# Optimization experiments

Hardware: AMD Instinct MI355X
Metric: run time of the kernel (lower is better)

Reference implementation:

```python
import jax, jax.numpy as jnp
import numpy as np
from jax import lax

K = 8          # num_classes
C_IN = 256     # in_channels
EPS = 1e-5


def resize_bilinear_ac(x, H, W):
    """Bilinear resize with align_corners=True. x: [B,C,h,w] -> [B,C,H,W]."""
    B, C, h, w = x.shape
    if h == H and w == W:
        return x
    ys = jnp.linspace(0.0, h - 1.0, H)
    xs = jnp.linspace(0.0, w - 1.0, W)
    y0 = jnp.floor(ys).astype(jnp.int32)
    x0 = jnp.floor(xs).astype(jnp.int32)
    y1 = jnp.minimum(y0 + 1, h - 1)
    x1 = jnp.minimum(x0 + 1, w - 1)
    wy = (ys - y0.astype(x.dtype))[None, None, :, None]
    wx = (xs - x0.astype(x.dtype))[None, None, None, :]
    g00 = x[:, :, y0][:, :, :, x0]
    g01 = x[:, :, y0][:, :, :, x1]
    g10 = x[:, :, y1][:, :, :, x0]
    g11 = x[:, :, y1][:, :, :, x1]
    top = g00 * (1.0 - wx) + g01 * wx
    bot = g10 * (1.0 - wx) + g11 * wx
    return top * (1.0 - wy) + bot * wy


def setup_inputs() -> dict:
    key = jax.random.key(0)
    ks = jax.random.split(key, 16)
    shapes = [(2, 256, 128, 128), (2, 256, 64, 64), (2, 256, 32, 32), (2, 256, 16, 16), (2, 256, 8, 8)]
    inp = {}
    for i, s in enumerate(shapes):
        inp[f"feat{i}"] = jax.random.normal(ks[i], s, dtype=jnp.float32)
    inp["attr_feat"] = jax.random.normal(ks[5], (2, K * C_IN, 64, 64), dtype=jnp.float32)
    # learned params
    inp["mlp_f_w"] = jax.random.normal(ks[6], (256, 256), dtype=jnp.float32) * 0.02
    inp["mlp_f_b"] = jnp.zeros((256,), dtype=jnp.float32)
    inp["mlp_a_w"] = jax.random.normal(ks[7], (256, 256), dtype=jnp.float32) * 0.02
    inp["mlp_a_b"] = jnp.zeros((256,), dtype=jnp.float32)
    # 5 grouped convs: [out=2048, in_per_group=256, 3, 3] each, no bias (BN follows)
    inp["conv_w"] = jax.random.normal(ks[8], (5, K * C_IN, C_IN, 3, 3), dtype=jnp.float32) * 0.02
    inp["bn_gamma"] = jnp.ones((5, K * C_IN), dtype=jnp.float32)
    inp["bn_beta"] = jnp.zeros((5, K * C_IN), dtype=jnp.float32)
    inp["bn_mean"] = jax.random.normal(ks[9], (5, K * C_IN), dtype=jnp.float32) * 0.1
    inp["bn_var"] = jax.random.uniform(ks[10], (5, K * C_IN), dtype=jnp.float32, minval=0.5, maxval=1.5)
    return inp


def _forward(feats, attr_feat, mlp_f_w, mlp_f_b, mlp_a_w, mlp_a_b, conv_w, bn_gamma, bn_beta, bn_mean, bn_var):
    B = attr_feat.shape[0]
    # global avg pool attr -> [B, K, C] -> mlp_a
    avg_attr = attr_feat.mean(axis=(2, 3)).reshape(B, K, C_IN)
    avg_attr = avg_attr @ mlp_a_w.T + mlp_a_b  # [B,K,256]
    outs = []
    for i, x in enumerate(feats):
        _, C, H, W = x.shape
        avg_x = x.mean(axis=(2, 3)) @ mlp_f_w.T + mlp_f_b          # [B,256]
        logits = jnp.einsum('bkc,bc->bk', avg_attr, avg_x)          # [B,K]
        attn = jax.nn.softmax(logits, axis=-1)
        y = resize_bilinear_ac(attr_feat, H, W)                      # [B,2048,H,W]
        y = lax.conv_general_dilated(
            y, conv_w[i], window_strides=(1, 1), padding=((1, 1), (1, 1)),
            dimension_numbers=('NCHW', 'OIHW', 'NCHW'), feature_group_count=K)
        inv = lax.rsqrt(bn_var[i] + EPS)
        y = (y - bn_mean[i][None, :, None, None]) * (inv * bn_gamma[i])[None, :, None, None] + bn_beta[i][None, :, None, None]
        y = jax.nn.relu(y)
        y = y.reshape(B, K, C, H, W)
        y = jnp.einsum('bkchw,bk->bchw', y, attn)                   # weighted sum over classes
        outs.append(jax.nn.relu(x + y))
    return tuple(outs)


def reference(feat0, feat1, feat2, feat3, feat4, attr_feat, mlp_f_w, mlp_f_b, mlp_a_w, mlp_a_b, conv_w, bn_gamma, bn_beta, bn_mean, bn_var):
    feats = [feat0, feat1, feat2, feat3, feat4]
    return _forward(feats, attr_feat, mlp_f_w, mlp_f_b, mlp_a_w, mlp_a_b, conv_w, bn_gamma, bn_beta, bn_mean, bn_var)
```

## Files before the change

kernel.cpp:

```cpp
#include <hip/hip_runtime.h>
#include <hip/hip_bf16.h>
#include <cstdint>

typedef __attribute__((ext_vector_type(8))) short short8;
typedef __attribute__((ext_vector_type(4))) float f32x4;

#define EPSV 1e-5f

__device__ __forceinline__ void gload_lds16(const void* g, void* l) {
  __builtin_amdgcn_global_load_lds(
      (const __attribute__((address_space(1))) void*)(uintptr_t)g,
      (__attribute__((address_space(3))) void*)(uint32_t)(uintptr_t)l,
      16, 0, 0);
}

__global__ void mean_kernel(const float* __restrict__ in, float* __restrict__ out,
                            int HW, float inv) {
  const int ch = blockIdx.x;
  const int t = threadIdx.x;
  const float* p = in + (size_t)ch * HW;
  float s = 0.f;
  const int nv = HW >> 2;
  const float4* pv = (const float4*)p;
  for (int i = t; i < nv; i += 256) { float4 v = pv[i]; s += v.x + v.y + v.z + v.w; }
  __shared__ float red[256];
  red[t] = s; __syncthreads();
  for (int off = 128; off > 0; off >>= 1) {
    if (t < off) red[t] += red[t + off];
    __syncthreads();
  }
  if (t == 0) out[ch] = red[0] * inv;
}

__global__ void wtrans_kernel(const float* __restrict__ cw,
                              const float* __restrict__ gamma, const float* __restrict__ beta,
                              const float* __restrict__ mean, const float* __restrict__ var,
                              __hip_bfloat16* __restrict__ wt, float* __restrict__ bias) {
  const int oc = blockIdx.x;
  const int i  = blockIdx.y;
  const int ci = threadIdx.x;
  const int idx = i * 2048 + oc;
  const float sc = rsqrtf(var[idx] + EPSV) * gamma[idx];
  if (ci == 0) bias[idx] = beta[idx] - mean[idx] * sc;
  const int g = oc >> 8, co = oc & 255;
  const float* src = cw + ((size_t)idx * 256 + ci) * 9;
  const size_t dbase = (size_t)(i * 8 + g) * 9 * 65536 + co * 256 + ci;
#pragma unroll
  for (int tap = 0; tap < 9; ++tap)
    wt[dbase + (size_t)tap * 65536] = __float2bfloat16(src[tap] * sc);
}

__global__ void gate_kernel(const float* __restrict__ meanA, const float* __restrict__ meanF,
                            const float* __restrict__ Wa, const float* __restrict__ ba,
                            const float* __restrict__ Wf, const float* __restrict__ bfp,
                            float* __restrict__ attn) {
  __shared__ float mA[16 * 256];
  __shared__ float mF[10 * 256];
  __shared__ float pA[16 * 256];
  __shared__ float pF[10 * 256];
  __shared__ float lg[80];
  const int t = threadIdx.x;
  for (int i = t; i < 4096; i += 256) mA[i] = meanA[i];
  for (int i = t; i < 2560; i += 256) mF[i] = meanF[i];
  __syncthreads();
  {
    float acc[16];
#pragma unroll
    for (int j = 0; j < 16; ++j) acc[j] = 0.f;
    for (int ci = 0; ci < 256; ++ci) {
      const float w = Wa[t * 256 + ci];
#pragma unroll
      for (int j = 0; j < 16; ++j) acc[j] += mA[j * 256 + ci] * w;
    }
    const float bb = ba[t];
#pragma unroll
    for (int j = 0; j < 16; ++j) pA[j * 256 + t] = acc[j] + bb;
  }
  {
    float acc[10];
#pragma unroll
    for (int j = 0; j < 10; ++j) acc[j] = 0.f;
    for (int ci = 0; ci < 256; ++ci) {
      const float w = Wf[t * 256 + ci];
#pragma unroll
      for (int j = 0; j < 10; ++j) acc[j] += mF[j * 256 + ci] * w;
    }
    const float bb = bfp[t];
#pragma unroll
    for (int j = 0; j < 10; ++j) pF[j * 256 + t] = acc[j] + bb;
  }
  __syncthreads();
  if (t < 80) {
    const int i = t >> 4, r = t & 15, b = r >> 3, k = r & 7;
    const float* a = &pA[(b * 8 + k) * 256];
    const float* f = &pF[(i * 2 + b) * 256];
    float d = 0.f;
    for (int c = 0; c < 256; ++c) d += a[c] * f[c];
    lg[t] = d;
  }
  __syncthreads();
  if (t < 10) {
    const int base = t * 8;
    float m = lg[base];
    for (int k = 1; k < 8; ++k) m = fmaxf(m, lg[base + k]);
    float e[8], s = 0.f;
    for (int k = 0; k < 8; ++k) { e[k] = __expf(lg[base + k] - m); s += e[k]; }
    const float invs = 1.f / s;
    for (int k = 0; k < 8; ++k) attn[base + k] = e[k] * invs;
  }
}

__global__ void resize_kernel(const float* __restrict__ attr,
                              __hip_bfloat16* __restrict__ R,
                              int W, int Hp, int Wp, float scl) {
  const int bk = blockIdx.x;
  const int yp = blockIdx.y;
  const int t  = threadIdx.x;
  const size_t rowbase = ((size_t)bk * Hp + yp) * (size_t)Wp * 256;
  if (yp == 0 || yp == Hp - 1) {
    uint32_t* p = (uint32_t*)(R + rowbase);
    const int n = Wp * 128;
    for (int idx = t; idx < n; idx += 256) p[idx] = 0u;
    return;
  }
  const int y = yp - 1;
  const float fy = y * scl;
  int y0 = (int)floorf(fy); if (y0 > 63) y0 = 63;
  const float wy = fy - (float)y0;
  const int y1 = min(y0 + 1, 63);
  __shared__ float buf[2][64][65];
  const int cc = t >> 2, seg = (t & 3) * 16;
  const int bb = bk >> 3, k = bk & 7;
  const float* ab = attr + (size_t)bb * 2048 * 4096;
  const int ci = t & 63;
  for (int cq = 0; cq < 4; ++cq) {
    __syncthreads();
    {
      const int ch = k * 256 + cq * 64 + cc;
      const float* r0 = ab + ((size_t)ch * 64 + y0) * 64;
      const float* r1 = ab + ((size_t)ch * 64 + y1) * 64;
#pragma unroll
      for (int u = 0; u < 4; ++u) {
        float4 v0 = ((const float4*)r0)[(t & 3) * 4 + u];
        float4 v1 = ((const float4*)r1)[(t & 3) * 4 + u];
        buf[0][cc][seg + u * 4 + 0] = v0.x; buf[0][cc][seg + u * 4 + 1] = v0.y;
        buf[0][cc][seg + u * 4 + 2] = v0.z; buf[0][cc][seg + u * 4 + 3] = v0.w;
        buf[1][cc][seg + u * 4 + 0] = v1.x; buf[1][cc][seg + u * 4 + 1] = v1.y;
        buf[1][cc][seg + u * 4 + 2] = v1.z; buf[1][cc][seg + u * 4 + 3] = v1.w;
      }
    }
    __syncthreads();
    for (int x = t >> 6; x < W; x += 4) {
      const float fx = x * scl;
      int x0 = (int)floorf(fx); if (x0 > 63) x0 = 63;
      const float wx = fx - (float)x0;
      const int x1 = min(x0 + 1, 63);
      const float top = buf[0][ci][x0] * (1.f - wx) + buf[0][ci][x1] * wx;
      const float bot = buf[1][ci][x0] * (1.f - wx) + buf[1][ci][x1] * wx;
      R[rowbase + (size_t)(x + 1) * 256 + cq * 64 + ci] = __float2bfloat16(top * (1.f - wy) + bot * wy);
    }
    if (t < 64) {
      R[rowbase + cq * 64 + t] = __float2bfloat16(0.f);
      R[rowbase + (size_t)(Wp - 1) * 256 + cq * 64 + t] = __float2bfloat16(0.f);
    }
  }
}

__device__ __forceinline__ void coords36(int u, int g0, int& g, int& ty, int& tx, int& cq) {
  g = g0 + u / 36;
  const int r = u % 36;
  const int tap = r >> 2;
  cq = r & 3;
  ty = tap / 3;
  tx = tap - ty * 3;
}

__global__ __launch_bounds__(256, 2)
void conv_kernel(const __hip_bfloat16* __restrict__ R,
                 const __hip_bfloat16* __restrict__ Wt,
                 const float* __restrict__ bias,
                 const float* __restrict__ attn,
                 const float* __restrict__ featp,
                 float* __restrict__ outp,
                 int W, int lw, int Hp, int Wp, int HW,
                 int b0, int NB, int gcount) {
  __shared__ alignas(16) __hip_bfloat16 ldsA[2][128 * 64];
  __shared__ alignas(16) __hip_bfloat16 ldsB[3][128 * 64];
  const int tid  = threadIdx.x;
  const int lane = tid & 63;
  const int wave = __builtin_amdgcn_readfirstlane(tid >> 6);
  const int wm = (wave >> 1) * 64;
  const int wn = (wave & 1) * 64;

  const int nx  = gridDim.x;
  const int lin = blockIdx.x;
  const int pos = ((nx & 7) == 0) ? ((lin & 7) * (nx >> 3) + (lin >> 3)) : lin;
  const int co0 = (pos & 1) * 128;
  const int n0  = (pos >> 1) * 128;

  const int bb  = (int)blockIdx.y % NB;
  const int gs  = (int)blockIdx.y / NB;
  const int b   = b0 + bb;
  const int g0  = gs * gcount;

  const int c8 = lane & 7;
  const int r8 = lane >> 3;
  int aoff[4], boff[4], dst[4];
#pragma unroll
  for (int q = 0; q < 4; ++q) {
    const int row = (wave * 4 + q) * 8 + r8;
    const int sc = (c8 ^ (row & 7)) << 3;
    aoff[q] = ((co0 + row) << 8) + sc;
    int sg = n0 + row; if (sg >= HW) sg = HW - 1;
    const int y = sg >> lw, x = sg & (W - 1);
    boff[q] = ((y * Wp + x) << 8) + sc;
    dst[q] = (wave * 4 + q) * 512;
  }

  const size_t rgstride = (size_t)Hp * Wp * 256;
  const __hip_bfloat16* Rb = R + (size_t)bb * 8 * rgstride;

  const f32x4 fz = {0.f, 0.f, 0.f, 0.f};
  f32x4 fin[4][4], acc[4][4];
#pragma unroll
  for (int mf = 0; mf < 4; ++mf)
#pragma unroll
    for (int nf = 0; nf < 4; ++nf) { fin[mf][nf] = fz; acc[mf][nf] = fz; }

  const int nstages = gcount * 36;

  {
    int g, ty, tx, cq;
    coords36(0, g0, g, ty, tx, cq);
    const __hip_bfloat16* wp = Wt + (((size_t)g * 9 + ty * 3 + tx) << 16) + (cq << 6);
    const __hip_bfloat16* rp = Rb + (size_t)g * rgstride + ((ty * Wp + tx) << 8) + (cq << 6);
#pragma unroll
    for (int q = 0; q < 4; ++q) gload_lds16(wp + aoff[q], &ldsA[0][dst[q]]);
#pragma unroll
    for (int q = 0; q < 4; ++q) gload_lds16(rp + boff[q], &ldsB[0][dst[q]]);
    coords36(1, g0, g, ty, tx, cq);
    const __hip_bfloat16* rp1 = Rb + (size_t)g * rgstride + ((ty * Wp + tx) << 8) + (cq << 6);
#pragma unroll
    for (int q = 0; q < 4; ++q) gload_lds16(rp1 + boff[q], &ldsB[1][dst[q]]);
  }

  int bcur = 0, b2 = 2;
  int foldc = 0, gcur = g0;

  for (int s = 0; s < nstages; ++s) {
    __builtin_amdgcn_s_barrier();
    asm volatile("" ::: "memory");
    if (s + 1 < nstages) {
      int g, ty, tx, cq;
      coords36(s + 1, g0, g, ty, tx, cq);
      const __hip_bfloat16* wp = Wt + (((size_t)g * 9 + ty * 3 + tx) << 16) + (cq << 6);
      __hip_bfloat16* dA = &ldsA[(s + 1) & 1][0];
#pragma unroll
      for (int q = 0; q < 4; ++q) gload_lds16(wp + aoff[q], dA + dst[q]);
    }
    if (s + 2 < nstages) {
      int g, ty, tx, cq;
      coords36(s + 2, g0, g, ty, tx, cq);
      const __hip_bfloat16* rp = Rb + (size_t)g * rgstride + ((ty * Wp + tx) << 8) + (cq << 6);
      __hip_bfloat16* dB = &ldsB[b2][0];
#pragma unroll
      for (int q = 0; q < 4; ++q) gload_lds16(rp + boff[q], dB + dst[q]);
    }
    if (s + 2 < nstages)      asm volatile("s_waitcnt vmcnt(12)" ::: "memory");
    else if (s + 1 < nstages) asm volatile("s_waitcnt vmcnt(8)" ::: "memory");
    else                      asm volatile("s_waitcnt vmcnt(0)" ::: "memory");
    __builtin_amdgcn_s_barrier();
    asm volatile("" ::: "memory");

    const __hip_bfloat16* pA = &ldsA[s & 1][0];
    const __hip_bfloat16* pB = &ldsB[bcur][0];
#pragma unroll
    for (int ks = 0; ks < 2; ++ks) {
      short8 af[4], bfv[4];
      const int cb = ks * 4 + (lane >> 4);
#pragma unroll
      for (int mf = 0; mf < 4; ++mf) {
        const int row = wm + mf * 16 + (lane & 15);
        af[mf] = *(const short8*)&pA[(row << 6) + ((cb ^ (row & 7)) << 3)];
      }
#pragma unroll
      for (int nf = 0; nf < 4; ++nf) {
        const int row = wn + nf * 16 + (lane & 15);
        bfv[nf] = *(const short8*)&pB[(row << 6) + ((cb ^ (row & 7)) << 3)];
      }
#pragma unroll
      for (int mf = 0; mf < 4; ++mf)
#pragma unroll
        for (int nf = 0; nf < 4; ++nf)
          acc[mf][nf] = __builtin_amdgcn_mfma_f32_16x16x32_bf16(
              af[mf], bfv[nf], acc[mf][nf], 0, 0, 0);
    }

    if (++bcur == 3) bcur = 0;
    if (++b2 == 3) b2 = 0;

    if (++foldc == 36) {
      foldc = 0;
      const float aw = attn[b * 8 + gcur];
#pragma unroll
      for (int mf = 0; mf < 4; ++mf) {
        const int cobase = co0 + wm + mf * 16 + ((lane >> 4) << 2);
#pragma unroll
        for (int r = 0; r < 4; ++r) {
          const float bs = bias[(gcur << 8) + cobase + r];
#pragma unroll
          for (int nf = 0; nf < 4; ++nf) {
            fin[mf][nf][r] += aw * fmaxf(acc[mf][nf][r] + bs, 0.f);
            acc[mf][nf][r] = 0.f;
          }
        }
      }
      ++gcur;
    }
  }

  const size_t plane = (size_t)256 * HW;
  if (featp) {
    const float* fb = featp + (size_t)b * plane;
    float* ob = outp + (size_t)b * plane;
#pragma unroll
    for (int mf = 0; mf < 4; ++mf) {
      const int cobase = co0 + wm + mf * 16 + ((lane >> 4) << 2);
#pragma unroll
      for (int nf = 0; nf < 4; ++nf) {
        const int n = n0 + wn + nf * 16 + (lane & 15);
        if (n < HW) {
#pragma unroll
          for (int r = 0; r < 4; ++r) {
            const size_t idx = (size_t)(cobase + r) * HW + n;
            ob[idx] = fmaxf(fb[idx] + fin[mf][nf][r], 0.f);
          }
        }
      }
    }
  } else {
    float* zb = outp + ((size_t)gs * 2 + b) * plane;
#pragma unroll
    for (int mf = 0; mf < 4; ++mf) {
      const int cobase = co0 + wm + mf * 16 + ((lane >> 4) << 2);
#pragma unroll
      for (int nf = 0; nf < 4; ++nf) {
        const int n = n0 + wn + nf * 16 + (lane & 15);
        if (n < HW) {
#pragma unroll
          for (int r = 0; r < 4; ++r)
            zb[(size_t)(cobase + r) * HW + n] = fin[mf][nf][r];
        }
      }
    }
  }
}

__global__ void reduce_kernel(const float* __restrict__ z, const float* __restrict__ feat,
                              float* __restrict__ outp, int total, int S) {
  const int idx = blockIdx.x * 256 + threadIdx.x;
  if (idx >= total) return;
  float s = feat[idx];
  for (int j = 0; j < S; ++j) s += z[(size_t)j * total + idx];
  outp[idx] = fmaxf(s, 0.f);
}

extern "C" void kernel_launch(void* const* d_in, const int* in_sizes, int n_in,
                              void* d_out, int out_size, void* d_ws, size_t ws_size,
                              hipStream_t stream) {
  const float* feat[5];
  for (int i = 0; i < 5; ++i) feat[i] = (const float*)d_in[i];
  const float* attr = (const float*)d_in[5];
  const float* mfw = (const float*)d_in[6];
  const float* mfb = (const float*)d_in[7];
  const float* maw = (const float*)d_in[8];
  const float* mab = (const float*)d_in[9];
  const float* cw  = (const float*)d_in[10];
  const float* bng = (const float*)d_in[11];
  const float* bnb = (const float*)d_in[12];
  const float* bnm = (const float*)d_in[13];
  const float* bnv = (const float*)d_in[14];
  float* out = (float*)d_out;

  char* ws = (char*)d_ws;
  float* attnW = (float*)(ws);
  float* meanA = (float*)(ws + 512);
  float* meanF = (float*)(ws + 20480);
  float* biasW = (float*)(ws + 32768);
  __hip_bfloat16* Wt = (__hip_bfloat16*)(ws + 131072);
  const size_t R_OFF = 47316992;
  __hip_bfloat16* Rbuf = (__hip_bfloat16*)(ws + R_OFF);

  const bool full = ws_size >= (size_t)219316224;
  const int NB = full ? 2 : 1;
  float* zbuf = (float*)(ws + R_OFF + (size_t)NB * 69222400);

  static const int HS[5] = {128, 64, 32, 16, 8};
  static const size_t OOFF[5] = {0, 8388608, 10485760, 11010048, 11141120};
  static const int SPLIT[5] = {1, 4, 8, 8, 8};

  mean_kernel<<<4096, 256, 0, stream>>>(attr, meanA, 4096, 1.f / 4096.f);
  for (int i = 0; i < 5; ++i) {
    const int HW = HS[i] * HS[i];
    mean_kernel<<<512, 256, 0, stream>>>(feat[i], meanF + i * 512, HW, 1.f / (float)HW);
  }
  wtrans_kernel<<<dim3(2048, 5), 256, 0, stream>>>(cw, bng, bnb, bnm, bnv, Wt, biasW);
  gate_kernel<<<1, 256, 0, stream>>>(meanA, meanF, maw, mab, mfw, mfb, attnW);

  for (int i = 0; i < 5; ++i) {
    const int H = HS[i], W = H, HW = H * W, Hp = H + 2, Wp = W + 2;
    const int lw = 31 - __builtin_clz((unsigned)W);
    const float scl = 63.f / (float)(H - 1);
    const int S = full ? SPLIT[i] : 1;
    const int gcount = 8 / S;
    const int ntiles = (HW + 127) / 128;
    for (int b0 = 0; b0 < 2; b0 += NB) {
      resize_kernel<<<dim3(NB * 8, Hp), 256, 0, stream>>>(
          attr + (size_t)b0 * 2048 * 4096, Rbuf, W, Hp, Wp, scl);
      const float* fp = (S == 1) ? feat[i] : nullptr;
      float* op = (S == 1) ? (out + OOFF[i]) : zbuf;
      conv_kernel<<<dim3(ntiles * 2, NB * S), 256, 0, stream>>>(
          Rbuf, Wt + (size_t)i * 8 * 9 * 65536, biasW + i * 2048, attnW + i * 16,
          fp, op, W, lw, Hp, Wp, HW, b0, NB, gcount);
    }
    if (S > 1) {
      const int total = 2 * 256 * HW;
      reduce_kernel<<<(total + 255) / 256, 256, 0, stream>>>(zbuf, feat[i], out + OOFF[i], total, S);
    }
  }
}
```

Baseline: 742.6 us.

## Load conv weight fragments straight into registers, double-buffer activation LDS

The weight (A) operand no longer goes through LDS. Each wave loads its MFMA A-fragments directly from global memory into registers with inline global_load_dwordx4, ping-ponging between two register sets across an unrolled pair of stages. The activation (B) tile drops from triple- to double-buffered LDS with a one-stage prefetch. This removes LDS traffic and footprint for A, but raises register pressure and leaves global latency hidden by only one stage of lookahead.

```diff
diff --git a/kernel.cpp b/kernel.cpp
--- a/kernel.cpp
+++ b/kernel.cpp
@@ -12,6 +12,14 @@
       (const __attribute__((address_space(1))) void*)(uintptr_t)g,
       (__attribute__((address_space(3))) void*)(uint32_t)(uintptr_t)l,
       16, 0, 0);
+}
+
+template <int OFF>
+__device__ __forceinline__ short8 aload(const __hip_bfloat16* sbase, uint32_t voff) {
+  short8 d;
+  asm volatile("global_load_dwordx4 %0, %1, %2 offset:%3"
+               : "=v"(d) : "v"(voff), "s"(sbase), "i"(OFF));
+  return d;
 }
 
 __global__ void mean_kernel(const float* __restrict__ in, float* __restrict__ out,
@@ -184,8 +192,7 @@
                  float* __restrict__ outp,
                  int W, int lw, int Hp, int Wp, int HW,
                  int b0, int NB, int gcount) {
-  __shared__ alignas(16) __hip_bfloat16 ldsA[2][128 * 64];
-  __shared__ alignas(16) __hip_bfloat16 ldsB[3][128 * 64];
+  __shared__ alignas(16) __hip_bfloat16 ldsB[2][128 * 64];
   const int tid  = threadIdx.x;
   const int lane = tid & 63;
   const int wave = __builtin_amdgcn_readfirstlane(tid >> 6);
@@ -205,17 +212,17 @@
 
   const int c8 = lane & 7;
   const int r8 = lane >> 3;
-  int aoff[4], boff[4], dst[4];
+  int boff[4], dst[4];
 #pragma unroll
   for (int q = 0; q < 4; ++q) {
     const int row = (wave * 4 + q) * 8 + r8;
     const int sc = (c8 ^ (row & 7)) << 3;
-    aoff[q] = ((co0 + row) << 8) + sc;
     int sg = n0 + row; if (sg >= HW) sg = HW - 1;
     const int y = sg >> lw, x = sg & (W - 1);
     boff[q] = ((y * Wp + x) << 8) + sc;
     dst[q] = (wave * 4 + q) * 512;
   }
+  const uint32_t voff = ((uint32_t)(co0 + wm + (lane & 15)) << 9) + ((lane >> 4) << 4);
 
   const size_t rgstride = (size_t)Hp * Wp * 256;
   const __hip_bfloat16* Rb = R + (size_t)bb * 8 * rgstride;
@@ -228,78 +235,71 @@
     for (int nf = 0; nf < 4; ++nf) { fin[mf][nf] = fz; acc[mf][nf] = fz; }
 
   const int nstages = gcount * 36;
+  short8 aP[8], aQ[8];
 
   {
-    int g, ty, tx, cq;
-    coords36(0, g0, g, ty, tx, cq);
-    const __hip_bfloat16* wp = Wt + (((size_t)g * 9 + ty * 3 + tx) << 16) + (cq << 6);
-    const __hip_bfloat16* rp = Rb + (size_t)g * rgstride + ((ty * Wp + tx) << 8) + (cq << 6);
-#pragma unroll
-    for (int q = 0; q < 4; ++q) gload_lds16(wp + aoff[q], &ldsA[0][dst[q]]);
+    const __hip_bfloat16* rp = Rb + (size_t)g0 * rgstride;
 #pragma unroll
     for (int q = 0; q < 4; ++q) gload_lds16(rp + boff[q], &ldsB[0][dst[q]]);
-    coords36(1, g0, g, ty, tx, cq);
-    const __hip_bfloat16* rp1 = Rb + (size_t)g * rgstride + ((ty * Wp + tx) << 8) + (cq << 6);
-#pragma unroll
-    for (int q = 0; q < 4; ++q) gload_lds16(rp1 + boff[q], &ldsB[1][dst[q]]);
-  }
-
-  int bcur = 0, b2 = 2;
+    const __hip_bfloat16* sA = Wt + ((size_t)g0 * 9 << 16);
+#pragma unroll
+    for (int mf = 0; mf < 4; ++mf) {
+      aP[mf * 2 + 0] = aload<0>(sA + mf * 4096, voff);
+      aP[mf * 2 + 1] = aload<64>(sA + mf * 4096, voff);
+    }
+  }
+
   int foldc = 0, gcur = g0;
 
-  for (int s = 0; s < nstages; ++s) {
-    __builtin_amdgcn_s_barrier();
-    asm volatile("" ::: "memory");
-    if (s + 1 < nstages) {
-      int g, ty, tx, cq;
-      coords36(s + 1, g0, g, ty, tx, cq);
-      const __hip_bfloat16* wp = Wt + (((size_t)g * 9 + ty * 3 + tx) << 16) + (cq << 6);
-      __hip_bfloat16* dA = &ldsA[(s + 1) & 1][0];
-#pragma unroll
-      for (int q = 0; q < 4; ++q) gload_lds16(wp + aoff[q], dA + dst[q]);
-    }
-    if (s + 2 < nstages) {
-      int g, ty, tx, cq;
-      coords36(s + 2, g0, g, ty, tx, cq);
-      const __hip_bfloat16* rp = Rb + (size_t)g * rgstride + ((ty * Wp + tx) << 8) + (cq << 6);
-      __hip_bfloat16* dB = &ldsB[b2][0];
-#pragma unroll
-      for (int q = 0; q < 4; ++q) gload_lds16(rp + boff[q], dB + dst[q]);
-    }
-    if (s + 2 < nstages)      asm volatile("s_waitcnt vmcnt(12)" ::: "memory");
-    else if (s + 1 < nstages) asm volatile("s_waitcnt vmcnt(8)" ::: "memory");
-    else                      asm volatile("s_waitcnt vmcnt(0)" ::: "memory");
-    __builtin_amdgcn_s_barrier();
-    asm volatile("" ::: "memory");
-
-    const __hip_bfloat16* pA = &ldsA[s & 1][0];
-    const __hip_bfloat16* pB = &ldsB[bcur][0];
-#pragma unroll
-    for (int ks = 0; ks < 2; ++ks) {
-      short8 af[4], bfv[4];
-      const int cb = ks * 4 + (lane >> 4);
-#pragma unroll
-      for (int mf = 0; mf < 4; ++mf) {
-        const int row = wm + mf * 16 + (lane & 15);
-        af[mf] = *(const short8*)&pA[(row << 6) + ((cb ^ (row & 7)) << 3)];
-      }
-#pragma unroll
-      for (int nf = 0; nf < 4; ++nf) {
-        const int row = wn + nf * 16 + (lane & 15);
-        bfv[nf] = *(const short8*)&pB[(row << 6) + ((cb ^ (row & 7)) << 3)];
-      }
-#pragma unroll
-      for (int mf = 0; mf < 4; ++mf)
-#pragma unroll
-        for (int nf = 0; nf < 4; ++nf)
-          acc[mf][nf] = __builtin_amdgcn_mfma_f32_16x16x32_bf16(
-              af[mf], bfv[nf], acc[mf][nf], 0, 0, 0);
-    }
-
-    if (++bcur == 3) bcur = 0;
-    if (++b2 == 3) b2 = 0;
-
-    if (++foldc == 36) {
+#define STAGE(s_, AUSE, ALOAD)                                                 \
+  {                                                                            \
+    __builtin_amdgcn_s_barrier();                                              \
+    asm volatile("" ::: "memory");                                             \
+    if ((s_) + 1 < nstages) {                                                  \
+      int g1, ty1, tx1, cq1;                                                   \
+      coords36((s_) + 1, g0, g1, ty1, tx1, cq1);                               \
+      const __hip_bfloat16* rp = Rb + (size_t)g1 * rgstride +                  \
+                                 ((ty1 * Wp + tx1) << 8) + (cq1 << 6);         \
+      __hip_bfloat16* dB = &ldsB[((s_) + 1) & 1][0];                           \
+      _Pragma("unroll")                                                        \
+      for (int q = 0; q < 4; ++q) gload_lds16(rp + boff[q], dB + dst[q]);      \
+      const __hip_bfloat16* sA =                                               \
+          Wt + (((size_t)g1 * 9 + ty1 * 3 + tx1) << 16) + (cq1 << 6);          \
+      _Pragma("unroll")                                                        \
+      for (int mf = 0; mf < 4; ++mf) {                                         \
+        ALOAD[mf * 2 + 0] = aload<0>(sA + mf * 4096, voff);                    \
+        ALOAD[mf * 2 + 1] = aload<64>(sA + mf * 4096, voff);                   \
+      }                                                                        \
+      asm volatile("s_waitcnt vmcnt(12)" ::: "memory");                        \
+    } else {                                                                   \
+      asm volatile("s_waitcnt vmcnt(0)" ::: "memory");                         \
+    }                                                                          \
+    __builtin_amdgcn_s_barrier();                                              \
+    asm volatile("" ::: "memory");                                             \
+    const __hip_bfloat16* pB = &ldsB[(s_) & 1][0];                             \
+    _Pragma("unroll")                                                          \
+    for (int ks = 0; ks < 2; ++ks) {                                           \
+      short8 bfv[4];                                                           \
+      const int cb = ks * 4 + (lane >> 4);                                     \
+      _Pragma("unroll")                                                        \
+      for (int nf = 0; nf < 4; ++nf) {                                         \
+        const int row = wn + nf * 16 + (lane & 15);                            \
+        bfv[nf] = *(const short8*)&pB[(row << 6) + ((cb ^ (row & 7)) << 3)];   \
+      }                                                                        \
+      _Pragma("unroll")                                                        \
+      for (int mf = 0; mf < 4; ++mf)                                           \
+        _Pragma("unroll")                                                      \
+        for (int nf = 0; nf < 4; ++nf)                                         \
+          acc[mf][nf] = __builtin_amdgcn_mfma_f32_16x16x32_bf16(               \
+              AUSE[mf * 2 + ks], bfv[nf], acc[mf][nf], 0, 0, 0);               \
+    }                                                                          \
+  }
+
+  for (int s = 0; s < nstages; s += 2) {
+    STAGE(s, aP, aQ);
+    STAGE(s + 1, aQ, aP);
+    foldc += 2;
+    if (foldc == 36) {
       foldc = 0;
       const float aw = attn[b * 8 + gcur];
 #pragma unroll
@@ -318,6 +318,7 @@
       ++gcur;
     }
   }
+#undef STAGE
 
   const size_t plane = (size_t)256 * HW;
   if (featp) {
```

Measured after the change: 1.136 ms. 53.0% more time.

## Add 256x256-tile conv kernel for large levels with bf16 split-K partials

Applied to the files above, without the earlier changes.

Adds a 512-thread conv kernel using 256x256 output tiles (all 256 output channels per block) with interleaved LDS prefetch, setprio around MFMA bursts, and accumulators folded into packed bf16 registers. It is used for the two largest pyramid levels with a class-group split (2 or 8), while smaller levels keep the old kernel split 8 ways. Split partial sums are now stored as bf16 instead of fp32, and the reduce kernel is vectorized over four elements per thread. This aims to raise arithmetic intensity per loaded tile and cut partial-sum traffic, at the cost of precision loss from bf16 intermediate accumulation and higher register pressure.

```diff
diff --git a/kernel.cpp b/kernel.cpp
--- a/kernel.cpp
+++ b/kernel.cpp
@@ -12,6 +12,12 @@
       (const __attribute__((address_space(1))) void*)(uintptr_t)g,
       (__attribute__((address_space(3))) void*)(uint32_t)(uintptr_t)l,
       16, 0, 0);
+}
+
+__device__ __forceinline__ uint32_t f2bf_rne(float v) {
+  const uint32_t u = __float_as_uint(v);
+  const uint32_t r = ((u >> 16) & 1u) + 0x7fffu;
+  return (u + r) >> 16;
 }
 
 __global__ void mean_kernel(const float* __restrict__ in, float* __restrict__ out,
@@ -175,13 +181,179 @@
   tx = tap - ty * 3;
 }
 
+__global__ __launch_bounds__(512, 1)
+void conv256_kernel(const __hip_bfloat16* __restrict__ R,
+                    const __hip_bfloat16* __restrict__ Wt,
+                    const float* __restrict__ bias,
+                    const float* __restrict__ attn,
+                    __hip_bfloat16* __restrict__ zout,
+                    int W, int lw, int Hp, int Wp, int HW,
+                    int NB, int gcount) {
+  __shared__ alignas(16) __hip_bfloat16 ldsA[2][256 * 64];
+  __shared__ alignas(16) __hip_bfloat16 ldsB[2][256 * 64];
+  const int tid  = threadIdx.x;
+  const int lane = tid & 63;
+  const int wave = __builtin_amdgcn_readfirstlane(tid >> 6);
+  const int wm = (wave >> 2) * 128;
+  const int wn = (wave & 3) * 64;
+
+  const int nx  = gridDim.x;
+  const int lin = blockIdx.x;
+  const int pos = ((nx & 7) == 0) ? ((lin & 7) * (nx >> 3) + (lin >> 3)) : lin;
+  const int n0  = pos * 256;
+
+  const int bb = (int)blockIdx.y % NB;
+  const int gs = (int)blockIdx.y / NB;
+  const int g0 = gs * gcount;
+
+  const int c8 = lane & 7, r8 = lane >> 3;
+  const int sc = (c8 ^ r8) << 3;
+  const int aoff0 = ((wave * 32 + r8) << 8) + sc;
+  const int dst0  = wave * 2048;
+  int boff[4];
+#pragma unroll
+  for (int q = 0; q < 4; ++q) {
+    const int row = wave * 32 + q * 8 + r8;
+    const int sg = n0 + row;
+    const int y = sg >> lw, x = sg & (W - 1);
+    boff[q] = ((y * Wp + x) << 8) + sc;
+  }
+
+  const size_t rgstride = (size_t)Hp * Wp * 256;
+  const __hip_bfloat16* Rb = R + (size_t)bb * 8 * rgstride;
+
+  const f32x4 fz = {0.f, 0.f, 0.f, 0.f};
+  f32x4 acc[8][4];
+  uint32_t finp[8][4][2];
+#pragma unroll
+  for (int mf = 0; mf < 8; ++mf)
+#pragma unroll
+    for (int nf = 0; nf < 4; ++nf) {
+      acc[mf][nf] = fz; finp[mf][nf][0] = 0u; finp[mf][nf][1] = 0u;
+    }
+
+  const int nk = gcount * 36;
+  {
+    const __hip_bfloat16* wp = Wt + ((size_t)g0 * 9 << 16);
+    const __hip_bfloat16* rp = Rb + (size_t)g0 * rgstride;
+#pragma unroll
+    for (int q = 0; q < 4; ++q) gload_lds16(wp + aoff0 + q * 2048, &ldsA[0][dst0 + q * 512]);
+#pragma unroll
+    for (int q = 0; q < 4; ++q) gload_lds16(rp + boff[q], &ldsB[0][dst0 + q * 512]);
+  }
+
+  int foldc = 0, gcur = g0;
+  for (int t = 0; t < nk; ++t) {
+    const int c = t & 1;
+    const bool pf = (t + 1 < nk);
+    int g1, ty1, tx1, cq1;
+    coords36(pf ? t + 1 : t, g0, g1, ty1, tx1, cq1);
+    const __hip_bfloat16* wp1 = Wt + (((size_t)g1 * 9 + ty1 * 3 + tx1) << 16) + (cq1 << 6);
+    const __hip_bfloat16* rp1 = Rb + (size_t)g1 * rgstride + ((ty1 * Wp + tx1) << 8) + (cq1 << 6);
+
+    asm volatile("s_waitcnt vmcnt(0)" ::: "memory");
+    __builtin_amdgcn_s_barrier();
+    asm volatile("" ::: "memory");
+
+    const __hip_bfloat16* pA = &ldsA[c][0];
+    const __hip_bfloat16* pB = &ldsB[c][0];
+    __hip_bfloat16* dA = &ldsA[c ^ 1][0];
+    __hip_bfloat16* dB = &ldsB[c ^ 1][0];
+
+#pragma unroll
+    for (int ks = 0; ks < 2; ++ks) {
+      const int cb = ks * 4 + (lane >> 4);
+      short8 bfv[4];
+#pragma unroll
+      for (int nf = 0; nf < 4; ++nf) {
+        const int row = wn + nf * 16 + (lane & 15);
+        bfv[nf] = *(const short8*)&pB[(row << 6) + ((cb ^ (row & 7)) << 3)];
+      }
+#pragma unroll
+      for (int h = 0; h < 2; ++h) {
+        short8 af[4];
+#pragma unroll
+        for (int m = 0; m < 4; ++m) {
+          const int row = wm + (h * 4 + m) * 16 + (lane & 15);
+          af[m] = *(const short8*)&pA[(row << 6) + ((cb ^ (row & 7)) << 3)];
+        }
+        if (ks == 0 && pf) {
+          if (h == 0) {
+#pragma unroll
+            for (int q = 0; q < 4; ++q) gload_lds16(wp1 + aoff0 + q * 2048, dA + dst0 + q * 512);
+          } else {
+#pragma unroll
+            for (int q = 0; q < 4; ++q) gload_lds16(rp1 + boff[q], dB + dst0 + q * 512);
+          }
+        }
+        __builtin_amdgcn_s_barrier();
+        __builtin_amdgcn_sched_barrier(0);
+        __builtin_amdgcn_s_setprio(1);
+#pragma unroll
+        for (int m = 0; m < 4; ++m)
+#pragma unroll
+          for (int nf = 0; nf < 4; ++nf)
+            acc[h * 4 + m][nf] = __builtin_amdgcn_mfma_f32_16x16x32_bf16(
+                af[m], bfv[nf], acc[h * 4 + m][nf], 0, 0, 0);
+        __builtin_amdgcn_s_setprio(0);
+        __builtin_amdgcn_s_barrier();
+        asm volatile("" ::: "memory");
+      }
+    }
+
+    if (++foldc == 36) {
+      foldc = 0;
+      const float aw = attn[bb * 8 + gcur];
+#pragma unroll
+      for (int mf = 0; mf < 8; ++mf) {
+        const int cobase = wm + mf * 16 + ((lane >> 4) << 2);
+#pragma unroll
+        for (int pr = 0; pr < 2; ++pr) {
+          const float b0v = bias[(gcur << 8) + cobase + pr * 2 + 0];
+          const float b1v = bias[(gcur << 8) + cobase + pr * 2 + 1];
+#pragma unroll
+          for (int nf = 0; nf < 4; ++nf) {
+            const uint32_t p = finp[mf][nf][pr];
+            const float f0 = __uint_as_float(p << 16)
+                           + aw * fmaxf(acc[mf][nf][pr * 2 + 0] + b0v, 0.f);
+            const float f1 = __uint_as_float(p & 0xffff0000u)
+                           + aw * fmaxf(acc[mf][nf][pr * 2 + 1] + b1v, 0.f);
+            finp[mf][nf][pr] = (f2bf_rne(f1) << 16) | f2bf_rne(f0);
+          }
+        }
+#pragma unroll
+        for (int nf = 0; nf < 4; ++nf) acc[mf][nf] = fz;
+      }
+      ++gcur;
+    }
+  }
+
+  __hip_bfloat16* zb = zout + (size_t)(gs * 2 + bb) * 256 * (size_t)HW;
+#pragma unroll
+  for (int mf = 0; mf < 8; ++mf) {
+    const int cobase = wm + mf * 16 + ((lane >> 4) << 2);
+#pragma unroll
+    for (int nf = 0; nf < 4; ++nf) {
+      const int n = n0 + wn + nf * 16 + (lane & 15);
+#pragma unroll
+      for (int pr = 0; pr < 2; ++pr) {
+        const uint32_t p = finp[mf][nf][pr];
+        zb[(size_t)(cobase + pr * 2 + 0) * HW + n] =
+            __float2bfloat16(__uint_as_float(p << 16));
+        zb[(size_t)(cobase + pr * 2 + 1) * HW + n] =
+            __float2bfloat16(__uint_as_float(p & 0xffff0000u));
+      }
+    }
+  }
+}
+
 __global__ __launch_bounds__(256, 2)
 void conv_kernel(const __hip_bfloat16* __restrict__ R,
                  const __hip_bfloat16* __restrict__ Wt,
                  const float* __restrict__ bias,
                  const float* __restrict__ attn,
                  const float* __restrict__ featp,
-                 float* __restrict__ outp,
+                 void* __restrict__ outp,
                  int W, int lw, int Hp, int Wp, int HW,
                  int b0, int NB, int gcount) {
   __shared__ alignas(16) __hip_bfloat16 ldsA[2][128 * 64];
@@ -228,7 +400,6 @@
     for (int nf = 0; nf < 4; ++nf) { fin[mf][nf] = fz; acc[mf][nf] = fz; }
 
   const int nstages = gcount * 36;
-
   {
     int g, ty, tx, cq;
     coords36(0, g0, g, ty, tx, cq);
@@ -238,7 +409,7 @@
     for (int q = 0; q < 4; ++q) gload_lds16(wp + aoff[q], &ldsA[0][dst[q]]);
 #pragma unroll
     for (int q = 0; q < 4; ++q) gload_lds16(rp + boff[q], &ldsB[0][dst[q]]);
-    coords36(1, g0, g, ty, tx, cq);
+    coords36(1 < nstages ? 1 : 0, g0, g, ty, tx, cq);
     const __hip_bfloat16* rp1 = Rb + (size_t)g * rgstride + ((ty * Wp + tx) << 8) + (cq << 6);
 #pragma unroll
     for (int q = 0; q < 4; ++q) gload_lds16(rp1 + boff[q], &ldsB[1][dst[q]]);
@@ -322,7 +493,7 @@
   const size_t plane = (size_t)256 * HW;
   if (featp) {
     const float* fb = featp + (size_t)b * plane;
-    float* ob = outp + (size_t)b * plane;
+    float* ob = (float*)outp + (size_t)b * plane;
 #pragma unroll
     for (int mf = 0; mf < 4; ++mf) {
       const int cobase = co0 + wm + mf * 16 + ((lane >> 4) << 2);
@@ -339,7 +510,7 @@
       }
     }
   } else {
-    float* zb = outp + ((size_t)gs * 2 + b) * plane;
+    __hip_bfloat16* zb = (__hip_bfloat16*)outp + ((size_t)gs * 2 + b) * plane;
 #pragma unroll
     for (int mf = 0; mf < 4; ++mf) {
       const int cobase = co0 + wm + mf * 16 + ((lane >> 4) << 2);
@@ -349,20 +520,29 @@
         if (n < HW) {
 #pragma unroll
           for (int r = 0; r < 4; ++r)
-            zb[(size_t)(cobase + r) * HW + n] = fin[mf][nf][r];
+            zb[(size_t)(cobase + r) * HW + n] = __float2bfloat16(fin[mf][nf][r]);
         }
       }
     }
   }
 }
 
-__global__ void reduce_kernel(const float* __restrict__ z, const float* __restrict__ feat,
+__global__ void reduce_kernel(const __hip_bfloat16* __restrict__ z,
+                              const float* __restrict__ feat,
                               float* __restrict__ outp, int total, int S) {
-  const int idx = blockIdx.x * 256 + threadIdx.x;
-  if (idx >= total) return;
-  float s = feat[idx];
-  for (int j = 0; j < S; ++j) s += z[(size_t)j * total + idx];
-  outp[idx] = fmaxf(s, 0.f);
+  const int i4 = (blockIdx.x * 256 + threadIdx.x) * 4;
+  if (i4 >= total) return;
+  float4 f = *(const float4*)(feat + i4);
+  float s0 = f.x, s1 = f.y, s2 = f.z, s3 = f.w;
+  for (int j = 0; j < S; ++j) {
+    const ushort4 v = *(const ushort4*)(z + (size_t)j * total + i4);
+    s0 += __uint_as_float((uint32_t)v.x << 16);
+    s1 += __uint_as_float((uint32_t)v.y << 16);
+    s2 += __uint_as_float((uint32_t)v.z << 16);
+    s3 += __uint_as_float((uint32_t)v.w << 16);
+  }
+  float4 o = {fmaxf(s0, 0.f), fmaxf(s1, 0.f), fmaxf(s2, 0.f), fmaxf(s3, 0.f)};
+  *(float4*)(outp + i4) = o;
 }
 
 extern "C" void kernel_launch(void* const* d_in, const int* in_sizes, int n_in,
@@ -393,11 +573,10 @@
 
   const bool full = ws_size >= (size_t)219316224;
   const int NB = full ? 2 : 1;
-  float* zbuf = (float*)(ws + R_OFF + (size_t)NB * 69222400);
+  __hip_bfloat16* zbuf = (__hip_bfloat16*)(ws + R_OFF + (size_t)NB * 69222400);
 
   static const int HS[5] = {128, 64, 32, 16, 8};
   static const size_t OOFF[5] = {0, 8388608, 10485760, 11010048, 11141120};
-  static const int SPLIT[5] = {1, 4, 8, 8, 8};
 
   mean_kernel<<<4096, 256, 0, stream>>>(attr, meanA, 4096, 1.f / 4096.f);
   for (int i = 0; i < 5; ++i) {
@@ -411,21 +590,36 @@
     const int H = HS[i], W = H, HW = H * W, Hp = H + 2, Wp = W + 2;
     const int lw = 31 - __builtin_clz((unsigned)W);
     const float scl = 63.f / (float)(H - 1);
-    const int S = full ? SPLIT[i] : 1;
-    const int gcount = 8 / S;
-    const int ntiles = (HW + 127) / 128;
-    for (int b0 = 0; b0 < 2; b0 += NB) {
-      resize_kernel<<<dim3(NB * 8, Hp), 256, 0, stream>>>(
-          attr + (size_t)b0 * 2048 * 4096, Rbuf, W, Hp, Wp, scl);
-      const float* fp = (S == 1) ? feat[i] : nullptr;
-      float* op = (S == 1) ? (out + OOFF[i]) : zbuf;
-      conv_kernel<<<dim3(ntiles * 2, NB * S), 256, 0, stream>>>(
-          Rbuf, Wt + (size_t)i * 8 * 9 * 65536, biasW + i * 2048, attnW + i * 16,
-          fp, op, W, lw, Hp, Wp, HW, b0, NB, gcount);
-    }
-    if (S > 1) {
-      const int total = 2 * 256 * HW;
-      reduce_kernel<<<(total + 255) / 256, 256, 0, stream>>>(zbuf, feat[i], out + OOFF[i], total, S);
-    }
-  }
-}
+
+    if (full) {
+      resize_kernel<<<dim3(16, Hp), 256, 0, stream>>>(attr, Rbuf, W, Hp, Wp, scl);
+      if (i <= 1) {
+        const int S = (i == 0) ? 2 : 8;
+        const int gcount = 8 / S;
+        conv256_kernel<<<dim3(HW / 256, 2 * S), 512, 0, stream>>>(
+            Rbuf, Wt + (size_t)i * 8 * 9 * 65536, biasW + i * 2048, attnW + i * 16,
+            zbuf, W, lw, Hp, Wp, HW, 2, gcount);
+        const int total = 2 * 256 * HW;
+        reduce_kernel<<<(total / 4 + 255) / 256, 256, 0, stream>>>(
+            zbuf, feat[i], out + OOFF[i], total, S);
+      } else {
+        const int ntiles = (HW + 127) / 128;
+        conv_kernel<<<dim3(ntiles * 2, 2 * 8), 256, 0, stream>>>(
+            Rbuf, Wt + (size_t)i * 8 * 9 * 65536, biasW + i * 2048, attnW + i * 16,
+            nullptr, zbuf, W, lw, Hp, Wp, HW, 0, 2, 1);
+        const int total = 2 * 256 * HW;
+        reduce_kernel<<<(total / 4 + 255) / 256, 256, 0, stream>>>(
+            zbuf, feat[i], out + OOFF[i], total, 8);
+      }
+    } else {
+      const int ntiles = (HW + 127) / 128;
+      for (int b0 = 0; b0 < 2; ++b0) {
+        resize_kernel<<<dim3(8, Hp), 256, 0, stream>>>(
+            attr + (size_t)b0 * 2048 * 4096, Rbuf, W, Hp, Wp, scl);
+        conv_kernel<<<dim3(ntiles * 2, 1), 256, 0, stream>>>(
+            Rbuf, Wt + (size_t)i * 8 * 9 * 65536, biasW + i * 2048, attnW + i * 16,
+            feat[i], out + OOFF[i], W, lw, Hp, Wp, HW, b0, 1, 8);
+      }
+    }
+  }
+}
```

New measurement: 723.9 us. 1.03x faster.
